# Performance work log

Hardware: AMD Instinct MI355X
Metric: run time of the kernel (lower is better)

Reference implementation:

```python
import jax, jax.numpy as jnp
import numpy as np

B, N, D = 16, 4096, 256
S = 8            # num_slots
ITERS = 3
H = 256          # mlp hidden = max(dim, 256)
SCALE = D ** -0.5
TEMP = 1.0
LN_EPS = 1e-5


def _ln(x, g, b):
    mu = jnp.mean(x, axis=-1, keepdims=True)
    var = jnp.var(x, axis=-1, keepdims=True)
    return (x - mu) * jax.lax.rsqrt(var + LN_EPS) * g + b


def setup_inputs() -> dict:
    key = jax.random.key(0)
    ks = jax.random.split(key, 16)
    xav = float(np.sqrt(6.0 / (S * D + D)))  # xavier_uniform over (1,S,D)
    lin = float(np.sqrt(1.0 / D))
    return {
        "embeddings": jax.random.normal(ks[0], (B, N, D), jnp.float32),
        "slots_noise": jax.random.normal(ks[1], (1, S, D), jnp.float32) * 0.0 + jax.random.normal(ks[1], (B, S, D), jnp.float32),
        "slots_mu": jax.random.uniform(ks[2], (1, S, D), jnp.float32, -xav, xav),
        "slots_logsigma": jax.random.uniform(ks[3], (1, S, D), jnp.float32, -xav, xav),
        "Wk": jax.random.uniform(ks[4], (S, D, D), jnp.float32, -lin, lin),
        "Wq": jax.random.uniform(ks[5], (D, D), jnp.float32, -lin, lin),
        "Wv": jax.random.uniform(ks[6], (S, D, D), jnp.float32, -lin, lin),
        "W_ih": jax.random.uniform(ks[7], (3 * D, D), jnp.float32, -lin, lin),
        "W_hh": jax.random.uniform(ks[8], (3 * D, D), jnp.float32, -lin, lin),
        "b_ih": jax.random.uniform(ks[9], (3 * D,), jnp.float32, -lin, lin),
        "b_hh": jax.random.uniform(ks[10], (3 * D,), jnp.float32, -lin, lin),
        "W1": jax.random.uniform(ks[11], (H, D), jnp.float32, -lin, lin),
        "b1": jnp.zeros((H,), jnp.float32),
        "W2": jax.random.uniform(ks[12], (D, H), jnp.float32, -float(np.sqrt(1.0 / H)), float(np.sqrt(1.0 / H))),
        "b2": jnp.zeros((D,), jnp.float32),
        "g_in": jnp.ones((D,), jnp.float32), "be_in": jnp.zeros((D,), jnp.float32),
        "g_s": jnp.ones((D,), jnp.float32), "be_s": jnp.zeros((D,), jnp.float32),
        "g_ff": jnp.ones((D,), jnp.float32), "be_ff": jnp.zeros((D,), jnp.float32),
    }


def _gru(x, h, W_ih, W_hh, b_ih, b_hh):
    # torch.nn.GRUCell math; x,h: [M, D]
    gi = x @ W_ih.T + b_ih
    gh = h @ W_hh.T + b_hh
    i_r, i_z, i_n = jnp.split(gi, 3, axis=-1)
    h_r, h_z, h_n = jnp.split(gh, 3, axis=-1)
    r = jax.nn.sigmoid(i_r + h_r)
    z = jax.nn.sigmoid(i_z + h_z)
    n = jnp.tanh(i_n + r * h_n)
    return (1.0 - z) * n + z * h


def reference(embeddings, slots_noise, slots_mu, slots_logsigma, Wk, Wq, Wv,
              W_ih, W_hh, b_ih, b_hh, W1, b1, W2, b2,
              g_in, be_in, g_s, be_s, g_ff, be_ff):
    b, n, d = embeddings.shape
    slots = slots_mu + jnp.exp(slots_logsigma) * slots_noise   # [B,S,D]
    emb = _ln(embeddings, g_in, be_in)                          # [B,N,D]
    # per-slot keys / values: keys[s] = emb @ Wk[s].T  -> [S,B,N,D]
    keys = jnp.einsum('bnd,sed->sbne', emb, Wk)
    values = jnp.einsum('bnd,sed->sbne', emb, Wv)

    attn_vis = None
    for _ in range(ITERS):
        slots_prev = slots
        slots_n = _ln(slots, g_s, be_s)
        q = jnp.einsum('bsd,ed->bse', slots_n, Wq)              # [B,S,D]
        dots = jnp.einsum('bsd,sbnd->bsn', q, keys) * SCALE     # [B,S,N]
        attn = jax.nn.softmax(dots / TEMP, axis=1)              # softmax over slots
        attn_vis = attn
        attn_w = attn / jnp.sum(attn, axis=-1, keepdims=True)   # normalize over tokens
        updates = jnp.einsum('sbnd,bsn->bsd', values, attn_w)   # [B,S,D]
        h = _gru(updates.reshape(b * S, d), slots_prev.reshape(b * S, d),
                 W_ih, W_hh, b_ih, b_hh).reshape(b, S, d)
        ff = _ln(h, g_ff, be_ff)
        slots = h + (jax.nn.relu(ff @ W1.T + b1) @ W2.T + b2)
    return slots, attn_vis
```

## Files before the change

kernel.cpp:

```cpp
#include <hip/hip_runtime.h>

#define DEVI __device__ __forceinline__

constexpr float SCALE = 0.0625f;
constexpr float LN_EPS = 1e-5f;

DEVI float dot256(const float* w, const float* x){
  float4 A = make_float4(0.f,0.f,0.f,0.f);
  #pragma unroll 8
  for (int k = 0; k < 64; ++k){
    float4 w4 = *(const float4*)(w + k*4);
    float4 x4 = *(const float4*)(x + k*4);
    A.x += w4.x*x4.x; A.y += w4.y*x4.y; A.z += w4.z*x4.z; A.w += w4.w*x4.w;
  }
  return (A.x+A.y)+(A.z+A.w);
}

DEVI float gemv_row(const float* __restrict__ W, const float4* __restrict__ xv4, int tid){
  const float4* wr = (const float4*)(W + (size_t)tid*256);
  float a0=0.f, a1=0.f, a2=0.f, a3=0.f;
  #pragma unroll 16
  for (int k = 0; k < 64; ++k){
    float4 w = wr[k];
    float4 x = xv4[k];
    a0 += w.x*x.x; a1 += w.y*x.y; a2 += w.z*x.z; a3 += w.w*x.w;
  }
  return (a0+a1)+(a2+a3);
}

DEVI float gemv_col(const float* __restrict__ W, const float4* __restrict__ xv4, int tid){
  const float* wc = W + tid;
  float a0=0.f, a1=0.f, a2=0.f, a3=0.f;
  #pragma unroll 8
  for (int e4 = 0; e4 < 64; ++e4){
    float4 x = xv4[e4];
    const float* p = wc + (size_t)e4*1024;
    a0 += x.x*p[0]; a1 += x.y*p[256]; a2 += x.z*p[512]; a3 += x.w*p[768];
  }
  return (a0+a1)+(a2+a3);
}

DEVI float block_ln(float x, const float* __restrict__ g, const float* __restrict__ be,
                    float* red, int tid, int lane, int wv){
  float v1 = x, v2 = x*x;
  #pragma unroll
  for (int o = 32; o; o >>= 1){ v1 += __shfl_xor(v1,o,64); v2 += __shfl_xor(v2,o,64); }
  if (lane == 0){ red[wv] = v1; red[4+wv] = v2; }
  __syncthreads();
  float mu = (red[0]+red[1]+red[2]+red[3]) * (1.f/256.f);
  float var = (red[4]+red[5]+red[6]+red[7]) * (1.f/256.f) - mu*mu;
  float inv = rsqrtf(var + LN_EPS);
  float r = (x - mu)*inv*g[tid] + be[tid];
  __syncthreads();
  return r;
}

DEVI void qproj(float sval, int r, int s, int tid,
                const float* __restrict__ g_s, const float* __restrict__ be_s,
                const float* __restrict__ Wq, const float* __restrict__ Wk,
                const float* __restrict__ g_in, const float* __restrict__ be_in,
                float* __restrict__ qg, float* __restrict__ gqbq,
                float4* xv4, float* red){
  float* xv = (float*)xv4;
  const int lane = tid & 63, wv = tid >> 6;
  float sn = block_ln(sval, g_s, be_s, red, tid, lane, wv);
  xv[tid] = sn;
  __syncthreads();
  float q = gemv_row(Wq, xv4, tid);
  __syncthreads();
  xv[tid] = q;
  __syncthreads();
  float qk = gemv_col(Wk + (size_t)s*65536, xv4, tid);
  float qgv = qk * g_in[tid] * SCALE;
  float bqv = qk * be_in[tid] * SCALE;
  qg[r*256 + tid] = qgv;
  float vq = qgv, vb = bqv;
  #pragma unroll
  for (int o = 32; o; o >>= 1){ vq += __shfl_xor(vq,o,64); vb += __shfl_xor(vb,o,64); }
  if (lane == 0){ red[wv] = vq; red[4+wv] = vb; }
  __syncthreads();
  if (tid == 0) gqbq[r*2+0] = red[0]+red[1]+red[2]+red[3];
  if (tid == 1) gqbq[r*2+1] = red[4]+red[5]+red[6]+red[7];
}

__global__ __launch_bounds__(256) void k_init_pre(const float* __restrict__ noise,
    const float* __restrict__ smu, const float* __restrict__ slsig,
    float* __restrict__ slotsA, float* __restrict__ uacc, float* __restrict__ Zacc,
    const float* __restrict__ g_s, const float* __restrict__ be_s,
    const float* __restrict__ Wq, const float* __restrict__ Wk,
    const float* __restrict__ g_in, const float* __restrict__ be_in,
    float* __restrict__ qg, float* __restrict__ gqbq,
    const float* __restrict__ W_ih, const float* __restrict__ Wv,
    float* __restrict__ Wf, float* __restrict__ Mt){
  __shared__ float SM[17408];
  const int tid = threadIdx.x, bid = blockIdx.x;

  if (bid < 128){
    float4* xv4 = (float4*)SM;
    float*  red = SM + 256;
    const int r = bid, s = r & 7;
    float sl = smu[s*256 + tid] + expf(slsig[s*256 + tid]) * noise[r*256 + tid];
    slotsA[r*256 + tid] = sl;
    uacc[r*256 + tid] = 0.f;
    if (tid == 0) Zacc[r] = 0.f;
    qproj(sl, r, s, tid, g_s, be_s, Wq, Wk, g_in, be_in, qg, gqbq, xv4, red);
    return;
  }

  float (*At)[68] = (float(*)[68])SM;
  float (*Bs)[68] = (float(*)[68])(SM + 128*68);
  const int gb = bid - 128;
  const bool isWf = gb < 384;
  const float *A, *B; float *C;
  int tile;
  if (isWf){
    int gm = gb >> 4; tile = gb & 15;
    A = W_ih + (size_t)(gm % 3) * 65536;
    B = Wv   + (size_t)(gm / 3) * 65536;
    C = Wf   + (size_t)gm * 65536;
  } else {
    int gm = (gb - 384) >> 4; tile = (gb - 384) & 15;
    A = Wk + (size_t)gm * 65536;
    B = Wq;
    C = Mt + (size_t)gm * 65536;
  }
  const int i0 = (tile >> 2) * 64, j0 = (tile & 3) * 64;
  const int ty = tid >> 4, tx = tid & 15;
  float acc[4][4];
  #pragma unroll
  for (int a = 0; a < 4; ++a)
    #pragma unroll
    for (int b = 0; b < 4; ++b) acc[a][b] = 0.f;

  for (int ko = 0; ko < 256; ko += 128){
    #pragma unroll
    for (int p = 0; p < 8; ++p){
      int idx4 = tid + p*256;
      int e = idx4 >> 4, jl4 = idx4 & 15;
      *(float4*)&Bs[e][jl4*4] = *(const float4*)(B + (size_t)(ko+e)*256 + j0 + jl4*4);
    }
    if (isWf){
      #pragma unroll
      for (int p = 0; p < 8; ++p){
        int idx4 = tid + p*256;
        int il = idx4 >> 5, e4 = idx4 & 31;
        float4 w = *(const float4*)(A + (size_t)(i0+il)*256 + ko + e4*4);
        At[e4*4+0][il] = w.x; At[e4*4+1][il] = w.y;
        At[e4*4+2][il] = w.z; At[e4*4+3][il] = w.w;
      }
    } else {
      #pragma unroll
      for (int p = 0; p < 8; ++p){
        int idx4 = tid + p*256;
        int e = idx4 >> 4, il4 = idx4 & 15;
        *(float4*)&At[e][il4*4] = *(const float4*)(A + (size_t)(ko+e)*256 + i0 + il4*4);
      }
    }
    __syncthreads();
    #pragma unroll 4
    for (int e = 0; e < 128; ++e){
      float4 a4 = *(const float4*)&At[e][ty*4];
      float4 b4 = *(const float4*)&Bs[e][tx*4];
      acc[0][0]+=a4.x*b4.x; acc[0][1]+=a4.x*b4.y; acc[0][2]+=a4.x*b4.z; acc[0][3]+=a4.x*b4.w;
      acc[1][0]+=a4.y*b4.x; acc[1][1]+=a4.y*b4.y; acc[1][2]+=a4.y*b4.z; acc[1][3]+=a4.y*b4.w;
      acc[2][0]+=a4.z*b4.x; acc[2][1]+=a4.z*b4.y; acc[2][2]+=a4.z*b4.z; acc[2][3]+=a4.z*b4.w;
      acc[3][0]+=a4.w*b4.x; acc[3][1]+=a4.w*b4.y; acc[3][2]+=a4.w*b4.z; acc[3][3]+=a4.w*b4.w;
    }
    __syncthreads();
  }
  #pragma unroll
  for (int ii = 0; ii < 4; ++ii)
    *(float4*)(C + (size_t)(i0+ty*4+ii)*256 + j0 + tx*4) =
      make_float4(acc[ii][0], acc[ii][1], acc[ii][2], acc[ii][3]);
}


__global__ __launch_bounds__(256) void k_gruF(const float* __restrict__ sin_,
    const float* __restrict__ uacc, const float* __restrict__ Zacc,
    const float* __restrict__ Wf, const float* __restrict__ b_ih,
    const float* __restrict__ ghb, float* __restrict__ hbuf){
  __shared__ float xs[16][260];
  __shared__ float ws[24][260];
  const int tid = threadIdx.x, bid = blockIdx.x;
  const int sg = bid >> 5, cgi = bid & 31, cbase = cgi * 8;
  #pragma unroll
  for (int i = 0; i < 4; ++i){
    int idx4 = tid + i*256, jj = idx4 >> 6, k4 = idx4 & 63;
    *(float4*)&xs[jj][k4*4] = *(const float4*)(uacc + ((size_t)(sg + 8*jj))*256 + k4*4);
  }
  #pragma unroll
  for (int i = 0; i < 6; ++i){
    int idx4 = tid + i*256, row = idx4 >> 6, k4 = idx4 & 63;
    int g = row >> 3, rr = row & 7;
    *(float4*)&ws[row][k4*4] =
      *(const float4*)(Wf + (size_t)(sg*3 + g)*65536 + ((size_t)(cbase + rr))*256 + k4*4);
  }
  __syncthreads();
  if (tid < 128){
    const int j = tid >> 3, cc = tid & 7, r = sg + 8*j, c = cbase + cc;
    float rZ = 1.f / Zacc[r];
    float ir_ = dot256(&ws[cc][0],    &xs[j][0]) * rZ + b_ih[c];
    float iz_ = dot256(&ws[8+cc][0],  &xs[j][0]) * rZ + b_ih[256 + c];
    float in_ = dot256(&ws[16+cc][0], &xs[j][0]) * rZ + b_ih[512 + c];
    float hr_ = ghb[((size_t)0*128 + r)*256 + c];
    float hz_ = ghb[((size_t)1*128 + r)*256 + c];
    float hn_ = ghb[((size_t)2*128 + r)*256 + c];
    float hp  = sin_[(size_t)r*256 + c];
    float rg = 1.f/(1.f + expf(-(ir_ + hr_)));
    float zg = 1.f/(1.f + expf(-(iz_ + hz_)));
    float ng = tanhf(in_ + rg*hn_);
    hbuf[(size_t)r*256 + c] = (1.f - zg)*ng + zg*hp;
  }
}

__global__ __launch_bounds__(256) void k_ffa(const float* __restrict__ hbuf,
    const float* __restrict__ g_ff, const float* __restrict__ be_ff,
    const float* __restrict__ W1, const float* __restrict__ b1,
    float* __restrict__ hid, float* __restrict__ uacc, float* __restrict__ Zacc){
  __shared__ float xs[16][260];
  __shared__ float ws[8][260];
  __shared__ float gA[256], gB[256];
  __shared__ float redA[16][17], redB[16][17];
  __shared__ float musL[16], invsL[16];
  const int tid = threadIdx.x, bid = blockIdx.x;
  const int sg = bid >> 5, cgi = bid & 31, cbase = cgi * 8;
  #pragma unroll
  for (int i = 0; i < 4; ++i){
    int idx4 = tid + i*256, jj = idx4 >> 6, k4 = idx4 & 63;
    *(float4*)&xs[jj][k4*4] = *(const float4*)(hbuf + ((size_t)(sg + 8*jj))*256 + k4*4);
  }
  #pragma unroll
  for (int i = 0; i < 2; ++i){
    int idx4 = tid + i*256, row = idx4 >> 6, k4 = idx4 & 63;
    *(float4*)&ws[row][k4*4] = *(const float4*)(W1 + ((size_t)(cbase + row))*256 + k4*4);
  }
  gA[tid] = g_ff[tid]; gB[tid] = be_ff[tid];
  __syncthreads();
  {
    int jr = tid >> 4, seg = tid & 15;
    float s1 = 0.f, s2 = 0.f;
    #pragma unroll
    for (int i = 0; i < 16; ++i){ float v = xs[jr][seg*16 + i]; s1 += v; s2 += v*v; }
    redA[jr][seg] = s1; redB[jr][seg] = s2;
    __syncthreads();
    if (tid < 16){
      float t1 = 0.f, t2 = 0.f;
      #pragma unroll
      for (int p = 0; p < 16; ++p){ t1 += redA[tid][p]; t2 += redB[tid][p]; }
      float mu = t1 * (1.f/256.f);
      float var = t2 * (1.f/256.f) - mu*mu;
      musL[tid] = mu; invsL[tid] = rsqrtf(var + LN_EPS);
    }
    __syncthreads();
    float mu = musL[jr], inv = invsL[jr];
    #pragma unroll
    for (int i = 0; i < 16; ++i){
      int k = seg*16 + i;
      xs[jr][k] = (xs[jr][k] - mu)*inv*gA[k] + gB[k];
    }
  }
  __syncthreads();
  if (tid < 128){
    const int j = tid >> 3, cc = tid & 7, r = sg + 8*j, c = cbase + cc;
    hid[(size_t)r*256 + c] = fmaxf(dot256(&ws[cc][0], &xs[j][0]) + b1[c], 0.f);
    uacc[(size_t)r*256 + c] = 0.f;
  }
  if (cgi == 0 && tid < 16) Zacc[sg + 8*tid] = 0.f;
}

__global__ __launch_bounds__(256) void k_ffb(const float* __restrict__ hid,
    const float* __restrict__ hbuf, const float* __restrict__ W2,
    const float* __restrict__ b2, float* __restrict__ sout,
    float* __restrict__ out_slots, float* __restrict__ gqbq, int last){
  __shared__ float xs[16][260];
  __shared__ float ws[8][260];
  const int tid = threadIdx.x, bid = blockIdx.x;
  const int sg = bid >> 5, cgi = bid & 31, cbase = cgi * 8;
  #pragma unroll
  for (int i = 0; i < 4; ++i){
    int idx4 = tid + i*256, jj = idx4 >> 6, k4 = idx4 & 63;
    *(float4*)&xs[jj][k4*4] = *(const float4*)(hid + ((size_t)(sg + 8*jj))*256 + k4*4);
  }
  #pragma unroll
  for (int i = 0; i < 2; ++i){
    int idx4 = tid + i*256, row = idx4 >> 6, k4 = idx4 & 63;
    *(float4*)&ws[row][k4*4] = *(const float4*)(W2 + ((size_t)(cbase + row))*256 + k4*4);
  }
  __syncthreads();
  if (tid < 128){
    const int j = tid >> 3, cc = tid & 7, r = sg + 8*j, c = cbase + cc;
    float out = hbuf[(size_t)r*256 + c] + dot256(&ws[cc][0], &xs[j][0]) + b2[c];
    sout[(size_t)r*256 + c] = out;
    if (last) out_slots[(size_t)r*256 + c] = out;
  }
  if (cgi == 0 && tid < 32)
    gqbq[(sg + 8*(tid>>1))*2 + (tid&1)] = 0.f;
}

__global__ __launch_bounds__(256) void k_lnqk(const float* __restrict__ sl,
    const float* __restrict__ g_s, const float* __restrict__ be_s,
    const float* __restrict__ Mt,
    const float* __restrict__ g_in, const float* __restrict__ be_in,
    float* __restrict__ qg, float* __restrict__ gqbq){
  __shared__ float xs[16][260];
  __shared__ float ws[8][260];
  __shared__ float gA[256], gB[256];
  __shared__ float redA[16][17], redB[16][17];
  __shared__ float musL[16], invsL[16];
  const int tid = threadIdx.x, bid = blockIdx.x;
  const int sg = bid >> 5, cgi = bid & 31, cbase = cgi * 8;
  #pragma unroll
  for (int i = 0; i < 4; ++i){
    int idx4 = tid + i*256, jj = idx4 >> 6, k4 = idx4 & 63;
    *(float4*)&xs[jj][k4*4] = *(const float4*)(sl + ((size_t)(sg + 8*jj))*256 + k4*4);
  }
  #pragma unroll
  for (int i = 0; i < 2; ++i){
    int idx4 = tid + i*256, row = idx4 >> 6, k4 = idx4 & 63;
    *(float4*)&ws[row][k4*4] =
      *(const float4*)(Mt + (size_t)sg*65536 + ((size_t)(cbase + row))*256 + k4*4);
  }
  gA[tid] = g_s[tid]; gB[tid] = be_s[tid];
  __syncthreads();
  {
    int jr = tid >> 4, seg = tid & 15;
    float s1 = 0.f, s2 = 0.f;
    #pragma unroll
    for (int i = 0; i < 16; ++i){ float v = xs[jr][seg*16 + i]; s1 += v; s2 += v*v; }
    redA[jr][seg] = s1; redB[jr][seg] = s2;
    __syncthreads();
    if (tid < 16){
      float t1 = 0.f, t2 = 0.f;
      #pragma unroll
      for (int p = 0; p < 16; ++p){ t1 += redA[tid][p]; t2 += redB[tid][p]; }
      float mu = t1 * (1.f/256.f);
      float var = t2 * (1.f/256.f) - mu*mu;
      musL[tid] = mu; invsL[tid] = rsqrtf(var + LN_EPS);
    }
    __syncthreads();
    float mu = musL[jr], inv = invsL[jr];
    #pragma unroll
    for (int i = 0; i < 16; ++i){
      int k = seg*16 + i;
      xs[jr][k] = (xs[jr][k] - mu)*inv*gA[k] + gB[k];
    }
  }
  __syncthreads();
  if (tid < 128){
    const int j = tid >> 3, cc = tid & 7, r = sg + 8*j, c = cbase + cc;
    float qk = dot256(&ws[cc][0], &xs[j][0]);
    float qgv = qk * g_in[c] * SCALE;
    float bqv = qk * be_in[c] * SCALE;
    qg[(size_t)r*256 + c] = qgv;
    float vq = qgv, vb = bqv;
    #pragma unroll
    for (int o = 1; o <= 4; o <<= 1){ vq += __shfl_xor(vq,o,64); vb += __shfl_xor(vb,o,64); }
    if (cc == 0){
      atomicAdd(&gqbq[r*2+0], vq);
      atomicAdd(&gqbq[r*2+1], vb);
    }
  }
}

__global__ __launch_bounds__(256) void k_main_gh(const float* __restrict__ emb,
    const float* __restrict__ qg, const float* __restrict__ gqbq,
    const float* __restrict__ g_in, const float* __restrict__ be_in,
    float* __restrict__ uacc, float* __restrict__ Zacc,
    float* __restrict__ out_attn, int write_attn,
    const float* __restrict__ sin_, const float* __restrict__ W_hh,
    const float* __restrict__ b_hh, float* __restrict__ ghb){
  __shared__ float U[8192];
  __shared__ float aL[512];
  __shared__ float red2[2][8][4];
  __shared__ float Zs[8], A2s[8], GqL[8], BqL[8];

  const int tid = threadIdx.x, lane = tid & 63, wv = tid >> 6;
  const int blk = blockIdx.x;

  if (blk >= 1024){
    float (*xs)[260]  = (float(*)[260])U;
    float (*wsh)[260] = (float(*)[260])(U + 16*260);
    const int idx = blk - 1024;
    const int g = idx >> 8, sub = idx & 255;
    const int sg = sub >> 5, cgi = sub & 31, cbase = cgi * 8;
    #pragma unroll
    for (int i = 0; i < 4; ++i){
      int idx4 = tid + i*256, jj = idx4 >> 6, k4 = idx4 & 63;
      *(float4*)&xs[jj][k4*4] = *(const float4*)(sin_ + ((size_t)(sg + 8*jj))*256 + k4*4);
    }
    #pragma unroll
    for (int i = 0; i < 2; ++i){
      int idx4 = tid + i*256, row = idx4 >> 6, k4 = idx4 & 63;
      *(float4*)&wsh[row][k4*4] =
        *(const float4*)(W_hh + (size_t)g*65536 + ((size_t)(cbase + row))*256 + k4*4);
    }
    __syncthreads();
    if (tid < 128){
      const int j = tid >> 3, cc = tid & 7, r = sg + 8*j, c = cbase + cc;
      ghb[((size_t)g*128 + r)*256 + c] = dot256(&wsh[cc][0], &xs[j][0]) + b_hh[g*256 + c];
    }
    return;
  }

  float* const qgL = U;
  float* const avL = U + 2048;
  float4* const Sp4 = (float4*)U;

  const int b = blk >> 6, tile = blk & 63;
  const int n0 = tile * 64;

  {
    const float4* src = (const float4*)(qg + (size_t)b * 2048);
    float4* dst = (float4*)qgL;
    #pragma unroll
    for (int k = 0; k < 2; ++k){
      int w = tid + k*256;
      int s = w >> 6, f = w & 63, qq = f >> 3, j = f & 7;
      dst[s*64 + qq*8 + ((j + qq) & 7)] = src[w];
    }
  }
  if (tid < 8){
    GqL[tid] = gqbq[(b*8 + tid)*2 + 0];
    BqL[tid] = gqbq[(b*8 + tid)*2 + 1];
  }
  __syncthreads();

  const int qq = tid & 7;
  float zsum[8], z2sum[8];
  #pragma unroll
  for (int s = 0; s < 8; ++s){ zsum[s] = 0.f; z2sum[s] = 0.f; }

  #pragma unroll
  for (int pass = 0; pass < 2; ++pass){
    const int t = pass*32 + (tid >> 3);
    const float4* xrow = (const float4*)(emb + ((size_t)(b*4096 + n0 + t))*256 + qq*32);
    float4 xv4[8];
    #pragma unroll
    for (int j = 0; j < 8; ++j) xv4[j] = xrow[j];
    float s1 = 0.f, s2 = 0.f, acc[8];
    #pragma unroll
    for (int s = 0; s < 8; ++s) acc[s] = 0.f;
    #pragma unroll
    for (int j = 0; j < 8; ++j){
      float4 u = xv4[j];
      s1 += (u.x+u.y)+(u.z+u.w);
      s2 += u.x*u.x+u.y*u.y+u.z*u.z+u.w*u.w;
      const float* qb = qgL + qq*32 + ((j + qq) & 7)*4;
      #pragma unroll
      for (int s = 0; s < 8; ++s){
        float4 q0 = *(const float4*)(qb + s*256);
        acc[s] += u.x*q0.x + u.y*q0.y + u.z*q0.z + u.w*q0.w;
      }
    }
    #pragma unroll
    for (int o = 1; o <= 4; o <<= 1){
      s1 += __shfl_xor(s1,o,64); s2 += __shfl_xor(s2,o,64);
      #pragma unroll
      for (int s = 0; s < 8; ++s) acc[s] += __shfl_xor(acc[s],o,64);
    }
    float mu = s1 * (1.f/256.f);
    float var = s2 * (1.f/256.f) - mu*mu;
    float inv = rsqrtf(var + LN_EPS);
    float dv[8], mx = -1e30f;
    #pragma unroll
    for (int s = 0; s < 8; ++s){
      dv[s] = inv * (acc[s] - mu * GqL[s]) + BqL[s];
      mx = fmaxf(mx, dv[s]);
    }
    float den = 0.f;
    #pragma unroll
    for (int s = 0; s < 8; ++s){ dv[s] = expf(dv[s] - mx); den += dv[s]; }
    float rden = 1.f / den;
    #pragma unroll
    for (int s = 0; s < 8; ++s){
      float at = dv[s] * rden;
      float av = at * inv;
      if (qq == 0){ avL[s*64 + t] = at; aL[s*64 + t] = av; }
      zsum[s] += at;
      z2sum[s] += av * mu;
    }
  }
  #pragma unroll
  for (int s = 0; s < 8; ++s){
    #pragma unroll
    for (int o = 32; o; o >>= 1){
      zsum[s] += __shfl_xor(zsum[s], o, 64);
      z2sum[s] += __shfl_xor(z2sum[s], o, 64);
    }
  }
  if (lane == 0){
    #pragma unroll
    for (int s = 0; s < 8; ++s){ red2[0][s][wv] = zsum[s]*0.125f; red2[1][s][wv] = z2sum[s]*0.125f; }
  }
  __syncthreads();
  if (tid < 8){
    Zs[tid]  = red2[0][tid][0]+red2[0][tid][1]+red2[0][tid][2]+red2[0][tid][3];
    A2s[tid] = red2[1][tid][0]+red2[1][tid][1]+red2[1][tid][2]+red2[1][tid][3];
  }
  if (write_attn){
    int s = tid >> 5, tk = tid & 31;
    #pragma unroll
    for (int p = 0; p < 2; ++p)
      out_attn[((size_t)(b*8 + s))*4096 + n0 + p*32 + tk] = avL[s*64 + p*32 + tk];
  }
  __syncthreads();
  {
    const int r4 = tid >> 6, cq = tid & 63;
    float4 S1[8];
    #pragma unroll
    for (int s = 0; s < 8; ++s) S1[s] = make_float4(0.f,0.f,0.f,0.f);
    const float4* xbase = (const float4*)(emb + ((size_t)(b*4096 + n0))*256) + cq;
    #pragma unroll 4
    for (int i = 0; i < 16; ++i){
      int t = r4 + i*4;
      float4 x4 = xbase[t*64];
      #pragma unroll
      for (int s = 0; s < 8; ++s){
        float a = aL[s*64 + t];
        S1[s].x += a*x4.x; S1[s].y += a*x4.y; S1[s].z += a*x4.z; S1[s].w += a*x4.w;
      }
    }
    #pragma unroll
    for (int s = 0; s < 8; ++s) Sp4[(r4*8 + s)*64 + cq] = S1[s];
  }
  __syncthreads();
  {
    const int c = tid;
    const float* Sp = (const float*)Sp4;
    float gc = g_in[c], bc = be_in[c];
    float* dst = uacc + ((size_t)b*8)*256 + c;
    #pragma unroll
    for (int si = 0; si < 8; ++si){
      int s = (si + blk) & 7;
      float v = Sp[(0*8+s)*256 + c] + Sp[(1*8+s)*256 + c]
              + Sp[(2*8+s)*256 + c] + Sp[(3*8+s)*256 + c];
      atomicAdd(&dst[s*256], gc * (v - A2s[s]) + bc * Zs[s]);
    }
    if (tid < 8) atomicAdd(&Zacc[b*8 + tid], Zs[tid]);
  }
}

extern "C" void kernel_launch(void* const* d_in, const int* in_sizes, int n_in,
                              void* d_out, int out_size, void* d_ws, size_t ws_size,
                              hipStream_t stream){
  const float* emb   = (const float*)d_in[0];
  const float* noise = (const float*)d_in[1];
  const float* smu   = (const float*)d_in[2];
  const float* slsig = (const float*)d_in[3];
  const float* Wk    = (const float*)d_in[4];
  const float* Wq    = (const float*)d_in[5];
  const float* Wv    = (const float*)d_in[6];
  const float* W_ih  = (const float*)d_in[7];
  const float* W_hh  = (const float*)d_in[8];
  const float* b_ih  = (const float*)d_in[9];
  const float* b_hh  = (const float*)d_in[10];
  const float* W1    = (const float*)d_in[11];
  const float* b1    = (const float*)d_in[12];
  const float* W2    = (const float*)d_in[13];
  const float* b2    = (const float*)d_in[14];
  const float* g_in  = (const float*)d_in[15];
  const float* be_in = (const float*)d_in[16];
  const float* g_s   = (const float*)d_in[17];
  const float* be_s  = (const float*)d_in[18];
  const float* g_ff  = (const float*)d_in[19];
  const float* be_ff = (const float*)d_in[20];

  float* ws     = (float*)d_ws;
  float* slotsA = ws;
  float* slotsB = ws + 32768;
  float* qg     = ws + 65536;
  float* gqbq   = ws + 98304;
  float* uacc   = ws + 98560;
  float* Zacc   = ws + 131328;
  float* ghb    = ws + 131456;
  float* hbuf   = ws + 229760;
  float* hid    = ws + 262528;
  float* Wf     = ws + 295296;
  float* Mt     = ws + 1868160;

  float* out_slots = (float*)d_out;
  float* out_attn  = out_slots + 32768;
  const int has_attn = (out_size >= 32768 + 16*8*4096);

  k_init_pre<<<dim3(640), dim3(256), 0, stream>>>(noise, smu, slsig, slotsA, uacc, Zacc,
      g_s, be_s, Wq, Wk, g_in, be_in, qg, gqbq, W_ih, Wv, Wf, Mt);
  for (int it = 0; it < 3; ++it){
    int last = (it == 2);
    float* sin  = (it == 1) ? slotsB : slotsA;
    float* sout = (it == 1) ? slotsA : slotsB;
    k_main_gh<<<dim3(1792), dim3(256), 0, stream>>>(emb, qg, gqbq, g_in, be_in,
        uacc, Zacc, out_attn, last && has_attn, sin, W_hh, b_hh, ghb);
    k_gruF<<<dim3(256), dim3(256), 0, stream>>>(sin, uacc, Zacc, Wf, b_ih, ghb, hbuf);
    k_ffa<<<dim3(256), dim3(256), 0, stream>>>(hbuf, g_ff, be_ff, W1, b1, hid, uacc, Zacc);
    k_ffb<<<dim3(256), dim3(256), 0, stream>>>(hid, hbuf, W2, b2, sout, out_slots,
        gqbq, last);
    if (!last)
      k_lnqk<<<dim3(256), dim3(256), 0, stream>>>(sout, g_s, be_s, Mt, g_in, be_in,
          qg, gqbq);
  }
}
```

Baseline: 323.1 us.

## Stage embedding tile in LDS, halve token tile, overlap weight precompute with main pass

```diff
diff --git a/kernel.cpp b/kernel.cpp
--- a/kernel.cpp
+++ b/kernel.cpp
@@ -55,15 +55,23 @@
   return r;
 }
 
-DEVI void qproj(float sval, int r, int s, int tid,
-                const float* __restrict__ g_s, const float* __restrict__ be_s,
-                const float* __restrict__ Wq, const float* __restrict__ Wk,
-                const float* __restrict__ g_in, const float* __restrict__ be_in,
-                float* __restrict__ qg, float* __restrict__ gqbq,
-                float4* xv4, float* red){
+__global__ __launch_bounds__(256) void k_initq(const float* __restrict__ noise,
+    const float* __restrict__ smu, const float* __restrict__ slsig,
+    float* __restrict__ slotsA, float* __restrict__ uacc, float* __restrict__ Zacc,
+    const float* __restrict__ g_s, const float* __restrict__ be_s,
+    const float* __restrict__ Wq, const float* __restrict__ Wk,
+    const float* __restrict__ g_in, const float* __restrict__ be_in,
+    float* __restrict__ qg, float* __restrict__ gqbq){
+  __shared__ float4 xv4[64];
+  __shared__ float red[8];
   float* xv = (float*)xv4;
+  const int r = blockIdx.x, tid = threadIdx.x, s = r & 7;
   const int lane = tid & 63, wv = tid >> 6;
-  float sn = block_ln(sval, g_s, be_s, red, tid, lane, wv);
+  float sl = smu[s*256 + tid] + expf(slsig[s*256 + tid]) * noise[r*256 + tid];
+  slotsA[r*256 + tid] = sl;
+  uacc[r*256 + tid] = 0.f;
+  if (tid == 0) Zacc[r] = 0.f;
+  float sn = block_ln(sl, g_s, be_s, red, tid, lane, wv);
   xv[tid] = sn;
   __syncthreads();
   float q = gemv_row(Wq, xv4, tid);
@@ -81,97 +89,6 @@
   __syncthreads();
   if (tid == 0) gqbq[r*2+0] = red[0]+red[1]+red[2]+red[3];
   if (tid == 1) gqbq[r*2+1] = red[4]+red[5]+red[6]+red[7];
-}
-
-__global__ __launch_bounds__(256) void k_init_pre(const float* __restrict__ noise,
-    const float* __restrict__ smu, const float* __restrict__ slsig,
-    float* __restrict__ slotsA, float* __restrict__ uacc, float* __restrict__ Zacc,
-    const float* __restrict__ g_s, const float* __restrict__ be_s,
-    const float* __restrict__ Wq, const float* __restrict__ Wk,
-    const float* __restrict__ g_in, const float* __restrict__ be_in,
-    float* __restrict__ qg, float* __restrict__ gqbq,
-    const float* __restrict__ W_ih, const float* __restrict__ Wv,
-    float* __restrict__ Wf, float* __restrict__ Mt){
-  __shared__ float SM[17408];
-  const int tid = threadIdx.x, bid = blockIdx.x;
-
-  if (bid < 128){
-    float4* xv4 = (float4*)SM;
-    float*  red = SM + 256;
-    const int r = bid, s = r & 7;
-    float sl = smu[s*256 + tid] + expf(slsig[s*256 + tid]) * noise[r*256 + tid];
-    slotsA[r*256 + tid] = sl;
-    uacc[r*256 + tid] = 0.f;
-    if (tid == 0) Zacc[r] = 0.f;
-    qproj(sl, r, s, tid, g_s, be_s, Wq, Wk, g_in, be_in, qg, gqbq, xv4, red);
-    return;
-  }
-
-  float (*At)[68] = (float(*)[68])SM;
-  float (*Bs)[68] = (float(*)[68])(SM + 128*68);
-  const int gb = bid - 128;
-  const bool isWf = gb < 384;
-  const float *A, *B; float *C;
-  int tile;
-  if (isWf){
-    int gm = gb >> 4; tile = gb & 15;
-    A = W_ih + (size_t)(gm % 3) * 65536;
-    B = Wv   + (size_t)(gm / 3) * 65536;
-    C = Wf   + (size_t)gm * 65536;
-  } else {
-    int gm = (gb - 384) >> 4; tile = (gb - 384) & 15;
-    A = Wk + (size_t)gm * 65536;
-    B = Wq;
-    C = Mt + (size_t)gm * 65536;
-  }
-  const int i0 = (tile >> 2) * 64, j0 = (tile & 3) * 64;
-  const int ty = tid >> 4, tx = tid & 15;
-  float acc[4][4];
-  #pragma unroll
-  for (int a = 0; a < 4; ++a)
-    #pragma unroll
-    for (int b = 0; b < 4; ++b) acc[a][b] = 0.f;
-
-  for (int ko = 0; ko < 256; ko += 128){
-    #pragma unroll
-    for (int p = 0; p < 8; ++p){
-      int idx4 = tid + p*256;
-      int e = idx4 >> 4, jl4 = idx4 & 15;
-      *(float4*)&Bs[e][jl4*4] = *(const float4*)(B + (size_t)(ko+e)*256 + j0 + jl4*4);
-    }
-    if (isWf){
-      #pragma unroll
-      for (int p = 0; p < 8; ++p){
-        int idx4 = tid + p*256;
-        int il = idx4 >> 5, e4 = idx4 & 31;
-        float4 w = *(const float4*)(A + (size_t)(i0+il)*256 + ko + e4*4);
-        At[e4*4+0][il] = w.x; At[e4*4+1][il] = w.y;
-        At[e4*4+2][il] = w.z; At[e4*4+3][il] = w.w;
-      }
-    } else {
-      #pragma unroll
-      for (int p = 0; p < 8; ++p){
-        int idx4 = tid + p*256;
-        int e = idx4 >> 4, il4 = idx4 & 15;
-        *(float4*)&At[e][il4*4] = *(const float4*)(A + (size_t)(ko+e)*256 + i0 + il4*4);
-      }
-    }
-    __syncthreads();
-    #pragma unroll 4
-    for (int e = 0; e < 128; ++e){
-      float4 a4 = *(const float4*)&At[e][ty*4];
-      float4 b4 = *(const float4*)&Bs[e][tx*4];
-      acc[0][0]+=a4.x*b4.x; acc[0][1]+=a4.x*b4.y; acc[0][2]+=a4.x*b4.z; acc[0][3]+=a4.x*b4.w;
-      acc[1][0]+=a4.y*b4.x; acc[1][1]+=a4.y*b4.y; acc[1][2]+=a4.y*b4.z; acc[1][3]+=a4.y*b4.w;
-      acc[2][0]+=a4.z*b4.x; acc[2][1]+=a4.z*b4.y; acc[2][2]+=a4.z*b4.z; acc[2][3]+=a4.z*b4.w;
-      acc[3][0]+=a4.w*b4.x; acc[3][1]+=a4.w*b4.y; acc[3][2]+=a4.w*b4.z; acc[3][3]+=a4.w*b4.w;
-    }
-    __syncthreads();
-  }
-  #pragma unroll
-  for (int ii = 0; ii < 4; ++ii)
-    *(float4*)(C + (size_t)(i0+ty*4+ii)*256 + j0 + tx*4) =
-      make_float4(acc[ii][0], acc[ii][1], acc[ii][2], acc[ii][3]);
 }
 
 
@@ -368,19 +285,90 @@
     float* __restrict__ uacc, float* __restrict__ Zacc,
     float* __restrict__ out_attn, int write_attn,
     const float* __restrict__ sin_, const float* __restrict__ W_hh,
-    const float* __restrict__ b_hh, float* __restrict__ ghb){
-  __shared__ float U[8192];
-  __shared__ float aL[512];
+    const float* __restrict__ b_hh, float* __restrict__ ghb,
+    const float* __restrict__ W_ih, const float* __restrict__ Wv,
+    const float* __restrict__ Wk, const float* __restrict__ Wq,
+    float* __restrict__ Wf, float* __restrict__ Mt){
+  __shared__ float SM[12288];
+  __shared__ float aL[256];
   __shared__ float red2[2][8][4];
   __shared__ float Zs[8], A2s[8], GqL[8], BqL[8];
 
   const int tid = threadIdx.x, lane = tid & 63, wv = tid >> 6;
   const int blk = blockIdx.x;
 
-  if (blk >= 1024){
-    float (*xs)[260]  = (float(*)[260])U;
-    float (*wsh)[260] = (float(*)[260])(U + 16*260);
-    const int idx = blk - 1024;
+  if (blk >= 2816){
+    float (*At)[68] = (float(*)[68])SM;
+    float (*Bs)[68] = (float(*)[68])(SM + 4352);
+    const int gb = blk - 2816;
+    const bool isWf = gb < 384;
+    const float *A, *B; float *C;
+    int tile;
+    if (isWf){
+      int gm = gb >> 4; tile = gb & 15;
+      A = W_ih + (size_t)(gm % 3) * 65536;
+      B = Wv   + (size_t)(gm / 3) * 65536;
+      C = Wf   + (size_t)gm * 65536;
+    } else {
+      int gm = (gb - 384) >> 4; tile = (gb - 384) & 15;
+      A = Wk + (size_t)gm * 65536;
+      B = Wq;
+      C = Mt + (size_t)gm * 65536;
+    }
+    const int i0 = (tile >> 2) * 64, j0 = (tile & 3) * 64;
+    const int ty = tid >> 4, tx = tid & 15;
+    float acc[4][4];
+    #pragma unroll
+    for (int a = 0; a < 4; ++a)
+      #pragma unroll
+      for (int b = 0; b < 4; ++b) acc[a][b] = 0.f;
+    for (int ko = 0; ko < 256; ko += 64){
+      #pragma unroll
+      for (int p = 0; p < 4; ++p){
+        int idx4 = tid + p*256;
+        int e = idx4 >> 4, jl4 = idx4 & 15;
+        *(float4*)&Bs[e][jl4*4] = *(const float4*)(B + (size_t)(ko+e)*256 + j0 + jl4*4);
+      }
+      if (isWf){
+        #pragma unroll
+        for (int p = 0; p < 4; ++p){
+          int idx4 = tid + p*256;
+          int il = idx4 >> 4, e4 = idx4 & 15;
+          float4 w = *(const float4*)(A + (size_t)(i0+il)*256 + ko + e4*4);
+          At[e4*4+0][il] = w.x; At[e4*4+1][il] = w.y;
+          At[e4*4+2][il] = w.z; At[e4*4+3][il] = w.w;
+        }
+      } else {
+        #pragma unroll
+        for (int p = 0; p < 4; ++p){
+          int idx4 = tid + p*256;
+          int e = idx4 >> 4, il4 = idx4 & 15;
+          *(float4*)&At[e][il4*4] = *(const float4*)(A + (size_t)(ko+e)*256 + i0 + il4*4);
+        }
+      }
+      __syncthreads();
+      #pragma unroll 4
+      for (int e = 0; e < 64; ++e){
+        float4 a4 = *(const float4*)&At[e][ty*4];
+        float4 b4 = *(const float4*)&Bs[e][tx*4];
+        acc[0][0]+=a4.x*b4.x; acc[0][1]+=a4.x*b4.y; acc[0][2]+=a4.x*b4.z; acc[0][3]+=a4.x*b4.w;
+        acc[1][0]+=a4.y*b4.x; acc[1][1]+=a4.y*b4.y; acc[1][2]+=a4.y*b4.z; acc[1][3]+=a4.y*b4.w;
+        acc[2][0]+=a4.z*b4.x; acc[2][1]+=a4.z*b4.y; acc[2][2]+=a4.z*b4.z; acc[2][3]+=a4.z*b4.w;
+        acc[3][0]+=a4.w*b4.x; acc[3][1]+=a4.w*b4.y; acc[3][2]+=a4.w*b4.z; acc[3][3]+=a4.w*b4.w;
+      }
+      __syncthreads();
+    }
+    #pragma unroll
+    for (int ii = 0; ii < 4; ++ii)
+      *(float4*)(C + (size_t)(i0+ty*4+ii)*256 + j0 + tx*4) =
+        make_float4(acc[ii][0], acc[ii][1], acc[ii][2], acc[ii][3]);
+    return;
+  }
+
+  if (blk >= 2048){
+    float (*xs)[260]  = (float(*)[260])SM;
+    float (*wsh)[260] = (float(*)[260])(SM + 4160);
+    const int idx = blk - 2048;
     const int g = idx >> 8, sub = idx & 255;
     const int sg = sub >> 5, cgi = sub & 31, cbase = cgi * 8;
     #pragma unroll
@@ -402,12 +390,13 @@
     return;
   }
 
-  float* const qgL = U;
-  float* const avL = U + 2048;
-  float4* const Sp4 = (float4*)U;
-
-  const int b = blk >> 6, tile = blk & 63;
-  const int n0 = tile * 64;
+  float* const tileL = SM;
+  float* const qgL = SM + 8192;
+  float* const avL = SM + 10240;
+  float4* const Sp4 = (float4*)(SM + 8192);
+
+  const int b = blk >> 7, tile = blk & 127;
+  const int n0 = tile * 32;
 
   {
     const float4* src = (const float4*)(qg + (size_t)b * 2048);
@@ -426,17 +415,21 @@
   __syncthreads();
 
   const int qq = tid & 7;
+  const int t  = tid >> 3;
   float zsum[8], z2sum[8];
   #pragma unroll
   for (int s = 0; s < 8; ++s){ zsum[s] = 0.f; z2sum[s] = 0.f; }
 
-  #pragma unroll
-  for (int pass = 0; pass < 2; ++pass){
-    const int t = pass*32 + (tid >> 3);
+  {
     const float4* xrow = (const float4*)(emb + ((size_t)(b*4096 + n0 + t))*256 + qq*32);
     float4 xv4[8];
     #pragma unroll
     for (int j = 0; j < 8; ++j) xv4[j] = xrow[j];
+    {
+      float4* tdst = (float4*)&tileL[t*256 + qq*32];
+      #pragma unroll
+      for (int j = 0; j < 8; ++j) tdst[j] = xv4[j];
+    }
     float s1 = 0.f, s2 = 0.f, acc[8];
     #pragma unroll
     for (int s = 0; s < 8; ++s) acc[s] = 0.f;
@@ -475,7 +468,7 @@
     for (int s = 0; s < 8; ++s){
       float at = dv[s] * rden;
       float av = at * inv;
-      if (qq == 0){ avL[s*64 + t] = at; aL[s*64 + t] = av; }
+      if (qq == 0){ avL[s*32 + t] = at; aL[s*32 + t] = av; }
       zsum[s] += at;
       z2sum[s] += av * mu;
     }
@@ -499,29 +492,26 @@
   }
   if (write_attn){
     int s = tid >> 5, tk = tid & 31;
-    #pragma unroll
-    for (int p = 0; p < 2; ++p)
-      out_attn[((size_t)(b*8 + s))*4096 + n0 + p*32 + tk] = avL[s*64 + p*32 + tk];
+    out_attn[((size_t)(b*8 + s))*4096 + n0 + tk] = avL[s*32 + tk];
   }
   __syncthreads();
   {
-    const int r4 = tid >> 6, cq = tid & 63;
-    float4 S1[8];
-    #pragma unroll
-    for (int s = 0; s < 8; ++s) S1[s] = make_float4(0.f,0.f,0.f,0.f);
-    const float4* xbase = (const float4*)(emb + ((size_t)(b*4096 + n0))*256) + cq;
+    const int r2 = tid >> 7, sh = (tid >> 6) & 1, cq = tid & 63;
+    float4 S1[4];
+    #pragma unroll
+    for (int so = 0; so < 4; ++so) S1[so] = make_float4(0.f,0.f,0.f,0.f);
     #pragma unroll 4
     for (int i = 0; i < 16; ++i){
-      int t = r4 + i*4;
-      float4 x4 = xbase[t*64];
-      #pragma unroll
-      for (int s = 0; s < 8; ++s){
-        float a = aL[s*64 + t];
-        S1[s].x += a*x4.x; S1[s].y += a*x4.y; S1[s].z += a*x4.z; S1[s].w += a*x4.w;
+      int tt = r2 + i*2;
+      float4 x4 = *(const float4*)&tileL[tt*256 + cq*4];
+      #pragma unroll
+      for (int so = 0; so < 4; ++so){
+        float a = aL[(sh*4+so)*32 + tt];
+        S1[so].x += a*x4.x; S1[so].y += a*x4.y; S1[so].z += a*x4.z; S1[so].w += a*x4.w;
       }
     }
     #pragma unroll
-    for (int s = 0; s < 8; ++s) Sp4[(r4*8 + s)*64 + cq] = S1[s];
+    for (int so = 0; so < 4; ++so) Sp4[(r2*8 + sh*4+so)*64 + cq] = S1[so];
   }
   __syncthreads();
   {
@@ -532,8 +522,7 @@
     #pragma unroll
     for (int si = 0; si < 8; ++si){
       int s = (si + blk) & 7;
-      float v = Sp[(0*8+s)*256 + c] + Sp[(1*8+s)*256 + c]
-              + Sp[(2*8+s)*256 + c] + Sp[(3*8+s)*256 + c];
+      float v = Sp[(0*8+s)*256 + c] + Sp[(1*8+s)*256 + c];
       atomicAdd(&dst[s*256], gc * (v - A2s[s]) + bc * Zs[s]);
     }
     if (tid < 8) atomicAdd(&Zacc[b*8 + tid], Zs[tid]);
@@ -582,14 +571,16 @@
   float* out_attn  = out_slots + 32768;
   const int has_attn = (out_size >= 32768 + 16*8*4096);
 
-  k_init_pre<<<dim3(640), dim3(256), 0, stream>>>(noise, smu, slsig, slotsA, uacc, Zacc,
-      g_s, be_s, Wq, Wk, g_in, be_in, qg, gqbq, W_ih, Wv, Wf, Mt);
+  k_initq<<<dim3(128), dim3(256), 0, stream>>>(noise, smu, slsig, slotsA, uacc, Zacc,
+      g_s, be_s, Wq, Wk, g_in, be_in, qg, gqbq);
   for (int it = 0; it < 3; ++it){
     int last = (it == 2);
     float* sin  = (it == 1) ? slotsB : slotsA;
     float* sout = (it == 1) ? slotsA : slotsB;
-    k_main_gh<<<dim3(1792), dim3(256), 0, stream>>>(emb, qg, gqbq, g_in, be_in,
-        uacc, Zacc, out_attn, last && has_attn, sin, W_hh, b_hh, ghb);
+    int grid = (it == 0) ? 3328 : 2816;
+    k_main_gh<<<dim3(grid), dim3(256), 0, stream>>>(emb, qg, gqbq, g_in, be_in,
+        uacc, Zacc, out_attn, last && has_attn, sin, W_hh, b_hh, ghb,
+        W_ih, Wv, Wk, Wq, Wf, Mt);
     k_gruF<<<dim3(256), dim3(256), 0, stream>>>(sin, uacc, Zacc, Wf, b_ih, ghb, hbuf);
     k_ffa<<<dim3(256), dim3(256), 0, stream>>>(hbuf, g_ff, be_ff, W1, b1, hid, uacc, Zacc);
     k_ffb<<<dim3(256), dim3(256), 0, stream>>>(hid, hbuf, W2, b2, sout, out_slots,
```

Result: slower. 361.9 us (+12.0%).

## Move weight-precompose GEMM blocks into first main-attention launch

Applied to the files above, without the earlier changes.

```diff
diff --git a/kernel.cpp b/kernel.cpp
--- a/kernel.cpp
+++ b/kernel.cpp
@@ -55,15 +55,23 @@
   return r;
 }
 
-DEVI void qproj(float sval, int r, int s, int tid,
-                const float* __restrict__ g_s, const float* __restrict__ be_s,
-                const float* __restrict__ Wq, const float* __restrict__ Wk,
-                const float* __restrict__ g_in, const float* __restrict__ be_in,
-                float* __restrict__ qg, float* __restrict__ gqbq,
-                float4* xv4, float* red){
+__global__ __launch_bounds__(256) void k_initq(const float* __restrict__ noise,
+    const float* __restrict__ smu, const float* __restrict__ slsig,
+    float* __restrict__ slotsA, float* __restrict__ uacc, float* __restrict__ Zacc,
+    const float* __restrict__ g_s, const float* __restrict__ be_s,
+    const float* __restrict__ Wq, const float* __restrict__ Wk,
+    const float* __restrict__ g_in, const float* __restrict__ be_in,
+    float* __restrict__ qg, float* __restrict__ gqbq){
+  __shared__ float4 xv4[64];
+  __shared__ float red[8];
   float* xv = (float*)xv4;
+  const int r = blockIdx.x, tid = threadIdx.x, s = r & 7;
   const int lane = tid & 63, wv = tid >> 6;
-  float sn = block_ln(sval, g_s, be_s, red, tid, lane, wv);
+  float sl = smu[s*256 + tid] + expf(slsig[s*256 + tid]) * noise[r*256 + tid];
+  slotsA[r*256 + tid] = sl;
+  uacc[r*256 + tid] = 0.f;
+  if (tid == 0) Zacc[r] = 0.f;
+  float sn = block_ln(sl, g_s, be_s, red, tid, lane, wv);
   xv[tid] = sn;
   __syncthreads();
   float q = gemv_row(Wq, xv4, tid);
@@ -81,97 +89,6 @@
   __syncthreads();
   if (tid == 0) gqbq[r*2+0] = red[0]+red[1]+red[2]+red[3];
   if (tid == 1) gqbq[r*2+1] = red[4]+red[5]+red[6]+red[7];
-}
-
-__global__ __launch_bounds__(256) void k_init_pre(const float* __restrict__ noise,
-    const float* __restrict__ smu, const float* __restrict__ slsig,
-    float* __restrict__ slotsA, float* __restrict__ uacc, float* __restrict__ Zacc,
-    const float* __restrict__ g_s, const float* __restrict__ be_s,
-    const float* __restrict__ Wq, const float* __restrict__ Wk,
-    const float* __restrict__ g_in, const float* __restrict__ be_in,
-    float* __restrict__ qg, float* __restrict__ gqbq,
-    const float* __restrict__ W_ih, const float* __restrict__ Wv,
-    float* __restrict__ Wf, float* __restrict__ Mt){
-  __shared__ float SM[17408];
-  const int tid = threadIdx.x, bid = blockIdx.x;
-
-  if (bid < 128){
-    float4* xv4 = (float4*)SM;
-    float*  red = SM + 256;
-    const int r = bid, s = r & 7;
-    float sl = smu[s*256 + tid] + expf(slsig[s*256 + tid]) * noise[r*256 + tid];
-    slotsA[r*256 + tid] = sl;
-    uacc[r*256 + tid] = 0.f;
-    if (tid == 0) Zacc[r] = 0.f;
-    qproj(sl, r, s, tid, g_s, be_s, Wq, Wk, g_in, be_in, qg, gqbq, xv4, red);
-    return;
-  }
-
-  float (*At)[68] = (float(*)[68])SM;
-  float (*Bs)[68] = (float(*)[68])(SM + 128*68);
-  const int gb = bid - 128;
-  const bool isWf = gb < 384;
-  const float *A, *B; float *C;
-  int tile;
-  if (isWf){
-    int gm = gb >> 4; tile = gb & 15;
-    A = W_ih + (size_t)(gm % 3) * 65536;
-    B = Wv   + (size_t)(gm / 3) * 65536;
-    C = Wf   + (size_t)gm * 65536;
-  } else {
-    int gm = (gb - 384) >> 4; tile = (gb - 384) & 15;
-    A = Wk + (size_t)gm * 65536;
-    B = Wq;
-    C = Mt + (size_t)gm * 65536;
-  }
-  const int i0 = (tile >> 2) * 64, j0 = (tile & 3) * 64;
-  const int ty = tid >> 4, tx = tid & 15;
-  float acc[4][4];
-  #pragma unroll
-  for (int a = 0; a < 4; ++a)
-    #pragma unroll
-    for (int b = 0; b < 4; ++b) acc[a][b] = 0.f;
-
-  for (int ko = 0; ko < 256; ko += 128){
-    #pragma unroll
-    for (int p = 0; p < 8; ++p){
-      int idx4 = tid + p*256;
-      int e = idx4 >> 4, jl4 = idx4 & 15;
-      *(float4*)&Bs[e][jl4*4] = *(const float4*)(B + (size_t)(ko+e)*256 + j0 + jl4*4);
-    }
-    if (isWf){
-      #pragma unroll
-      for (int p = 0; p < 8; ++p){
-        int idx4 = tid + p*256;
-        int il = idx4 >> 5, e4 = idx4 & 31;
-        float4 w = *(const float4*)(A + (size_t)(i0+il)*256 + ko + e4*4);
-        At[e4*4+0][il] = w.x; At[e4*4+1][il] = w.y;
-        At[e4*4+2][il] = w.z; At[e4*4+3][il] = w.w;
-      }
-    } else {
-      #pragma unroll
-      for (int p = 0; p < 8; ++p){
-        int idx4 = tid + p*256;
-        int e = idx4 >> 4, il4 = idx4 & 15;
-        *(float4*)&At[e][il4*4] = *(const float4*)(A + (size_t)(ko+e)*256 + i0 + il4*4);
-      }
-    }
-    __syncthreads();
-    #pragma unroll 4
-    for (int e = 0; e < 128; ++e){
-      float4 a4 = *(const float4*)&At[e][ty*4];
-      float4 b4 = *(const float4*)&Bs[e][tx*4];
-      acc[0][0]+=a4.x*b4.x; acc[0][1]+=a4.x*b4.y; acc[0][2]+=a4.x*b4.z; acc[0][3]+=a4.x*b4.w;
-      acc[1][0]+=a4.y*b4.x; acc[1][1]+=a4.y*b4.y; acc[1][2]+=a4.y*b4.z; acc[1][3]+=a4.y*b4.w;
-      acc[2][0]+=a4.z*b4.x; acc[2][1]+=a4.z*b4.y; acc[2][2]+=a4.z*b4.z; acc[2][3]+=a4.z*b4.w;
-      acc[3][0]+=a4.w*b4.x; acc[3][1]+=a4.w*b4.y; acc[3][2]+=a4.w*b4.z; acc[3][3]+=a4.w*b4.w;
-    }
-    __syncthreads();
-  }
-  #pragma unroll
-  for (int ii = 0; ii < 4; ++ii)
-    *(float4*)(C + (size_t)(i0+ty*4+ii)*256 + j0 + tx*4) =
-      make_float4(acc[ii][0], acc[ii][1], acc[ii][2], acc[ii][3]);
 }
 
 
@@ -368,8 +285,11 @@
     float* __restrict__ uacc, float* __restrict__ Zacc,
     float* __restrict__ out_attn, int write_attn,
     const float* __restrict__ sin_, const float* __restrict__ W_hh,
-    const float* __restrict__ b_hh, float* __restrict__ ghb){
-  __shared__ float U[8192];
+    const float* __restrict__ b_hh, float* __restrict__ ghb,
+    const float* __restrict__ W_ih, const float* __restrict__ Wv,
+    const float* __restrict__ Wk, const float* __restrict__ Wq,
+    float* __restrict__ Wf, float* __restrict__ Mt){
+  __shared__ float U[8704];
   __shared__ float aL[512];
   __shared__ float red2[2][8][4];
   __shared__ float Zs[8], A2s[8], GqL[8], BqL[8];
@@ -377,9 +297,77 @@
   const int tid = threadIdx.x, lane = tid & 63, wv = tid >> 6;
   const int blk = blockIdx.x;
 
+  if (blk >= 1792){
+    float (*At)[68] = (float(*)[68])U;
+    float (*Bs)[68] = (float(*)[68])(U + 4352);
+    const int gb = blk - 1792;
+    const bool isWf = gb < 384;
+    const float *A, *B; float *C;
+    int tile;
+    if (isWf){
+      int gm = gb >> 4; tile = gb & 15;
+      A = W_ih + (size_t)(gm % 3) * 65536;
+      B = Wv   + (size_t)(gm / 3) * 65536;
+      C = Wf   + (size_t)gm * 65536;
+    } else {
+      int gm = (gb - 384) >> 4; tile = (gb - 384) & 15;
+      A = Wk + (size_t)gm * 65536;
+      B = Wq;
+      C = Mt + (size_t)gm * 65536;
+    }
+    const int i0 = (tile >> 2) * 64, j0 = (tile & 3) * 64;
+    const int ty = tid >> 4, tx = tid & 15;
+    float acc[4][4];
+    #pragma unroll
+    for (int a = 0; a < 4; ++a)
+      #pragma unroll
+      for (int b = 0; b < 4; ++b) acc[a][b] = 0.f;
+    for (int ko = 0; ko < 256; ko += 64){
+      #pragma unroll
+      for (int p = 0; p < 4; ++p){
+        int idx4 = tid + p*256;
+        int e = idx4 >> 4, jl4 = idx4 & 15;
+        *(float4*)&Bs[e][jl4*4] = *(const float4*)(B + (size_t)(ko+e)*256 + j0 + jl4*4);
+      }
+      if (isWf){
+        #pragma unroll
+        for (int p = 0; p < 4; ++p){
+          int idx4 = tid + p*256;
+          int il = idx4 >> 4, e4 = idx4 & 15;
+          float4 w = *(const float4*)(A + (size_t)(i0+il)*256 + ko + e4*4);
+          At[e4*4+0][il] = w.x; At[e4*4+1][il] = w.y;
+          At[e4*4+2][il] = w.z; At[e4*4+3][il] = w.w;
+        }
+      } else {
+        #pragma unroll
+        for (int p = 0; p < 4; ++p){
+          int idx4 = tid + p*256;
+          int e = idx4 >> 4, il4 = idx4 & 15;
+          *(float4*)&At[e][il4*4] = *(const float4*)(A + (size_t)(ko+e)*256 + i0 + il4*4);
+        }
+      }
+      __syncthreads();
+      #pragma unroll 4
+      for (int e = 0; e < 64; ++e){
+        float4 a4 = *(const float4*)&At[e][ty*4];
+        float4 b4 = *(const float4*)&Bs[e][tx*4];
+        acc[0][0]+=a4.x*b4.x; acc[0][1]+=a4.x*b4.y; acc[0][2]+=a4.x*b4.z; acc[0][3]+=a4.x*b4.w;
+        acc[1][0]+=a4.y*b4.x; acc[1][1]+=a4.y*b4.y; acc[1][2]+=a4.y*b4.z; acc[1][3]+=a4.y*b4.w;
+        acc[2][0]+=a4.z*b4.x; acc[2][1]+=a4.z*b4.y; acc[2][2]+=a4.z*b4.z; acc[2][3]+=a4.z*b4.w;
+        acc[3][0]+=a4.w*b4.x; acc[3][1]+=a4.w*b4.y; acc[3][2]+=a4.w*b4.z; acc[3][3]+=a4.w*b4.w;
+      }
+      __syncthreads();
+    }
+    #pragma unroll
+    for (int ii = 0; ii < 4; ++ii)
+      *(float4*)(C + (size_t)(i0+ty*4+ii)*256 + j0 + tx*4) =
+        make_float4(acc[ii][0], acc[ii][1], acc[ii][2], acc[ii][3]);
+    return;
+  }
+
   if (blk >= 1024){
     float (*xs)[260]  = (float(*)[260])U;
-    float (*wsh)[260] = (float(*)[260])(U + 16*260);
+    float (*wsh)[260] = (float(*)[260])(U + 4160);
     const int idx = blk - 1024;
     const int g = idx >> 8, sub = idx & 255;
     const int sg = sub >> 5, cgi = sub & 31, cbase = cgi * 8;
@@ -582,14 +570,16 @@
   float* out_attn  = out_slots + 32768;
   const int has_attn = (out_size >= 32768 + 16*8*4096);
 
-  k_init_pre<<<dim3(640), dim3(256), 0, stream>>>(noise, smu, slsig, slotsA, uacc, Zacc,
-      g_s, be_s, Wq, Wk, g_in, be_in, qg, gqbq, W_ih, Wv, Wf, Mt);
+  k_initq<<<dim3(128), dim3(256), 0, stream>>>(noise, smu, slsig, slotsA, uacc, Zacc,
+      g_s, be_s, Wq, Wk, g_in, be_in, qg, gqbq);
   for (int it = 0; it < 3; ++it){
     int last = (it == 2);
     float* sin  = (it == 1) ? slotsB : slotsA;
     float* sout = (it == 1) ? slotsA : slotsB;
-    k_main_gh<<<dim3(1792), dim3(256), 0, stream>>>(emb, qg, gqbq, g_in, be_in,
-        uacc, Zacc, out_attn, last && has_attn, sin, W_hh, b_hh, ghb);
+    int grid = (it == 0) ? 2304 : 1792;
+    k_main_gh<<<dim3(grid), dim3(256), 0, stream>>>(emb, qg, gqbq, g_in, be_in,
+        uacc, Zacc, out_attn, last && has_attn, sin, W_hh, b_hh, ghb,
+        W_ih, Wv, Wk, Wq, Wf, Mt);
     k_gruF<<<dim3(256), dim3(256), 0, stream>>>(sin, uacc, Zacc, Wf, b_ih, ghb, hbuf);
     k_ffa<<<dim3(256), dim3(256), 0, stream>>>(hbuf, g_ff, be_ff, W1, b1, hid, uacc, Zacc);
     k_ffb<<<dim3(256), dim3(256), 0, stream>>>(hid, hbuf, W2, b2, sout, out_slots,
```

After: 326.9 us. About the same (+1.2%).
